# Performance work log

Hardware: AMD Instinct MI355X
Metric: run time of the kernel (lower is better)

Reference implementation:

```python
import jax, jax.numpy as jnp
import numpy as np

N = 100000      # physical-network nodes
E = 3200000     # directed edges (avg degree 32)
DIN = 128       # input_dim
DH = 128        # embedding_dim
DOUT = 128      # output_dim
NUM_GRAPHS = 1


def setup_inputs() -> dict:
    key = jax.random.key(0)
    ks = jax.random.split(key, 8)
    s = 0.05
    x = jax.random.normal(ks[0], (N, DIN), dtype=jnp.float32)
    edge_index = jax.random.randint(ks[1], (2, E), 0, N, dtype=jnp.int64)
    W1 = jax.random.normal(ks[2], (DIN, DH), dtype=jnp.float32) * s
    b1 = jnp.zeros((DH,), dtype=jnp.float32)
    W2 = jax.random.normal(ks[3], (DH, DH), dtype=jnp.float32) * s
    b2 = jnp.zeros((DH,), dtype=jnp.float32)
    W3 = jax.random.normal(ks[4], (DH, DOUT), dtype=jnp.float32) * s
    b3 = jnp.zeros((DOUT,), dtype=jnp.float32)
    return {"x": x, "edge_index": edge_index,
            "W1": W1, "b1": b1, "W2": W2, "b2": b2, "W3": W3, "b3": b3}


def _gcn_norm(edge_index, n_nodes):
    # PyG GCNConv default: add self-loops, symmetric D^{-1/2} (A+I) D^{-1/2} norm.
    loops = jnp.arange(n_nodes, dtype=edge_index.dtype)
    src = jnp.concatenate([edge_index[0], loops])   # [E+N]
    dst = jnp.concatenate([edge_index[1], loops])   # [E+N]
    deg = jax.ops.segment_sum(jnp.ones_like(dst, dtype=jnp.float32), dst,
                              num_segments=n_nodes)
    dinv = jax.lax.rsqrt(deg)  # deg >= 1 because of self-loops
    norm = dinv[src] * dinv[dst]                    # [E+N]
    return src, dst, norm


def _gcn_conv(h, W, b, src, dst, norm, n_nodes):
    h = h @ W                                       # [N, dout] linear first (PyG order)
    msg = h[src] * norm[:, None]                    # gather + edge scaling
    agg = jax.ops.segment_sum(msg, dst, num_segments=n_nodes)  # scatter-add
    return agg + b


def reference(x, edge_index, W1, b1, W2, b2, W3, b3):
    src, dst, norm = _gcn_norm(edge_index, N)
    h = jax.nn.relu(_gcn_conv(x, W1, b1, src, dst, norm, N))
    # dropout is identity in eval mode
    h = jax.nn.relu(_gcn_conv(h, W2, b2, src, dst, norm, N))
    h = _gcn_conv(h, W3, b3, src, dst, norm, N)
    return h.reshape(NUM_GRAPHS, N // NUM_GRAPHS, -1)
```

## Files before the change

kernel.cpp:

```cpp
#include <hip/hip_runtime.h>
#include <cstddef>
#include <cstdint>

#define NN 100000
#define NE 3200000
#define D  128
#define NB 782
#define BSH 7
#define NPB 512
#define CHUNK 6250

typedef short v8s __attribute__((ext_vector_type(8)));
typedef float v4f __attribute__((ext_vector_type(4)));


__device__ __forceinline__ unsigned short f2bf(float f) {
  uint32_t u = __float_as_uint(f);
  uint32_t r = u + 0x7fff + ((u >> 16) & 1);
  return (unsigned short)(r >> 16);
}
__device__ __forceinline__ float bf_lo(uint32_t v) {
  return __uint_as_float(v << 16);
}
__device__ __forceinline__ float bf_hi(uint32_t v) {
  return __uint_as_float(v & 0xffff0000u);
}


__global__ void k_zero(int* __restrict__ p, int n) {
  int i = blockIdx.x * 256 + threadIdx.x;
  if (i < n) p[i] = 0;
}

__global__ __launch_bounds__(256) void kb_count(const int* __restrict__ dst,
                                                int* __restrict__ gb) {
  __shared__ int h[NB];
  for (int i = threadIdx.x; i < NB; i += 256) h[i] = 0;
  __syncthreads();
  int lo = blockIdx.x * CHUNK, hi = lo + CHUNK;
  if (hi > NE) hi = NE;
  for (int e = lo + threadIdx.x; e < hi; e += 256)
    atomicAdd(&h[dst[e] >> BSH], 1);
  __syncthreads();
  for (int i = threadIdx.x; i < NB; i += 256)
    if (h[i]) atomicAdd(&gb[i], h[i]);
}

__global__ __launch_bounds__(1024) void kb_scan(const int* __restrict__ gb,
                                                int* __restrict__ boff,
                                                int* __restrict__ gcur) {
  __shared__ int s[1024];
  int t = threadIdx.x;
  int v = (t < NB) ? gb[t] : 0;
  s[t] = v;
  __syncthreads();
  for (int d = 1; d < 1024; d <<= 1) {
    int u = (t >= d) ? s[t - d] : 0;
    __syncthreads();
    s[t] += u;
    __syncthreads();
  }
  if (t < NB) {
    int x = s[t] - v;
    boff[t] = x;
    gcur[t] = x;
  }
  if (t == 0) boff[NB] = NE;
}

__global__ __launch_bounds__(256) void kb_part(const int* __restrict__ src,
                                               const int* __restrict__ dst,
                                               int* __restrict__ gcur,
                                               uint2* __restrict__ ebuf) {
  __shared__ int h[NB];
  __shared__ int cur[NB];
  for (int i = threadIdx.x; i < NB; i += 256) h[i] = 0;
  __syncthreads();
  int lo = blockIdx.x * CHUNK, hi = lo + CHUNK;
  if (hi > NE) hi = NE;
  for (int e = lo + threadIdx.x; e < hi; e += 256)
    atomicAdd(&h[dst[e] >> BSH], 1);
  __syncthreads();
  for (int i = threadIdx.x; i < NB; i += 256)
    cur[i] = h[i] ? atomicAdd(&gcur[i], h[i]) : 0;
  __syncthreads();
  for (int e = lo + threadIdx.x; e < hi; e += 256) {
    int s = src[e], d = dst[e];
    int p = atomicAdd(&cur[d >> BSH], 1);
    ebuf[p] = make_uint2((unsigned)s, (unsigned)d);
  }
}

__global__ __launch_bounds__(256) void kb_nodecnt(const uint2* __restrict__ ebuf,
                                                  const int* __restrict__ boff,
                                                  int* __restrict__ cnt) {
  int b = blockIdx.x;
  __shared__ int h[128];
  if (threadIdx.x < 128) h[threadIdx.x] = 0;
  __syncthreads();
  int lo = boff[b], hi = boff[b + 1];
  for (int e = lo + threadIdx.x; e < hi; e += 256)
    atomicAdd(&h[ebuf[e].y & 127], 1);
  __syncthreads();
  int node = b * 128 + threadIdx.x;
  if (threadIdx.x < 128 && node < NN) cnt[node] = h[threadIdx.x];
}

__global__ void k_dinv(const int* __restrict__ cnt, float* __restrict__ dinv) {
  int i = blockIdx.x * 256 + threadIdx.x;
  if (i < NN) dinv[i] = rsqrtf((float)(cnt[i] + 1));
}

__global__ void k_scan1(const int* __restrict__ cnt, int* __restrict__ tmp,
                        int* __restrict__ part) {
  __shared__ int s[256];
  int i = blockIdx.x * 256 + threadIdx.x;
  int v = (i < NN) ? cnt[i] : 0;
  s[threadIdx.x] = v;
  __syncthreads();
  for (int d = 1; d < 256; d <<= 1) {
    int t = (threadIdx.x >= d) ? s[threadIdx.x - d] : 0;
    __syncthreads();
    s[threadIdx.x] += t;
    __syncthreads();
  }
  if (i < NN) tmp[i] = s[threadIdx.x] - v;
  if (threadIdx.x == 255) part[blockIdx.x] = s[255];
}

__global__ void k_scan2(int* __restrict__ part, int nb) {
  __shared__ int s[512];
  int v = (threadIdx.x < nb) ? part[threadIdx.x] : 0;
  s[threadIdx.x] = v;
  __syncthreads();
  for (int d = 1; d < 512; d <<= 1) {
    int t = (threadIdx.x >= d) ? s[threadIdx.x - d] : 0;
    __syncthreads();
    s[threadIdx.x] += t;
    __syncthreads();
  }
  if (threadIdx.x < nb) part[threadIdx.x] = s[threadIdx.x] - v;
}

__global__ void k_scan3(const int* __restrict__ tmp, const int* __restrict__ part,
                        int* __restrict__ row_off) {
  int i = blockIdx.x * 256 + threadIdx.x;
  if (i < NN) row_off[i] = tmp[i] + part[blockIdx.x];
  if (blockIdx.x == 0 && threadIdx.x == 0) row_off[NN] = NE;
}

__global__ __launch_bounds__(256) void kb_fill(const uint2* __restrict__ ebuf,
                                               const int* __restrict__ boff,
                                               const int* __restrict__ row_off,
                                               int* __restrict__ col) {
  int b = blockIdx.x;
  __shared__ int cur[128];
  int node = b * 128 + threadIdx.x;
  if (threadIdx.x < 128) cur[threadIdx.x] = (node < NN) ? row_off[node] : 0;
  __syncthreads();
  int lo = boff[b], hi = boff[b + 1];
  for (int e = lo + threadIdx.x; e < hi; e += 256) {
    uint2 p = ebuf[e];
    int pos = atomicAdd(&cur[p.y & 127], 1);
    col[pos] = (int)p.x;
  }
}


__global__ void k_wt(const float* __restrict__ W, unsigned short* __restrict__ wt) {
  int idx = blockIdx.x * 256 + threadIdx.x;
  if (idx >= 16384) return;
  int k = idx >> 7, c = idx & 127;
  float w = W[idx];
  unsigned short hi = f2bf(w);
  float wh = __uint_as_float((uint32_t)hi << 16);
  unsigned short lo = f2bf(w - wh);
  wt[(size_t)c * 128 + k] = hi;
  wt[16384 + (size_t)c * 128 + k] = lo;
}


__global__ void k_cvt(const float* __restrict__ x, unsigned short* __restrict__ xb) {
  const int n4 = NN * D / 4;
  for (int i = blockIdx.x * 256 + threadIdx.x; i < n4; i += gridDim.x * 256) {
    float4 v = ((const float4*)x)[i];
    uint2 o;
    o.x = (uint32_t)f2bf(v.x) | ((uint32_t)f2bf(v.y) << 16);
    o.y = (uint32_t)f2bf(v.z) | ((uint32_t)f2bf(v.w) << 16);
    ((uint2*)xb)[i] = o;
  }
}


__global__ __launch_bounds__(256) void k_gemm_mfma(
    const unsigned short* __restrict__ A, const unsigned short* __restrict__ wt,
    const float* __restrict__ dinv, unsigned short* __restrict__ C) {
  const int wave = threadIdx.x >> 6;
  const int lane = threadIdx.x & 63;
  const int row0 = blockIdx.x * 128 + wave * 32;
  const int rl = lane & 15;
  const int kg = lane >> 4;

  v4f acc[2][8];
#pragma unroll
  for (int t = 0; t < 2; ++t)
#pragma unroll
    for (int ct = 0; ct < 8; ++ct) acc[t][ct] = (v4f){0.f, 0.f, 0.f, 0.f};

  union U { uint4 u; v8s v; };

#pragma unroll
  for (int ks = 0; ks < 4; ++ks) {
    U a[2];
#pragma unroll
    for (int t = 0; t < 2; ++t) {
      int r = row0 + t * 16 + rl;
      if (r >= NN) r = NN - 1;
      a[t].u = *(const uint4*)(A + (size_t)r * D + ks * 32 + kg * 8);
    }
#pragma unroll
    for (int ct = 0; ct < 8; ++ct) {
      U bh, bl;
      size_t wo = (size_t)(ct * 16 + rl) * 128 + ks * 32 + kg * 8;
      bh.u = *(const uint4*)(wt + wo);
      bl.u = *(const uint4*)(wt + 16384 + wo);
      acc[0][ct] = __builtin_amdgcn_mfma_f32_16x16x32_bf16(a[0].v, bh.v, acc[0][ct], 0, 0, 0);
      acc[1][ct] = __builtin_amdgcn_mfma_f32_16x16x32_bf16(a[1].v, bh.v, acc[1][ct], 0, 0, 0);
      acc[0][ct] = __builtin_amdgcn_mfma_f32_16x16x32_bf16(a[0].v, bl.v, acc[0][ct], 0, 0, 0);
      acc[1][ct] = __builtin_amdgcn_mfma_f32_16x16x32_bf16(a[1].v, bl.v, acc[1][ct], 0, 0, 0);
    }
  }

#pragma unroll
  for (int t = 0; t < 2; ++t) {
#pragma unroll
    for (int i = 0; i < 4; ++i) {
      int row = row0 + t * 16 + kg * 4 + i;
      if (row < NN) {
        float dv = dinv[row];
#pragma unroll
        for (int ct = 0; ct < 8; ++ct)
          C[(size_t)row * D + ct * 16 + rl] = f2bf(dv * acc[t][ct][i]);
      }
    }
  }
}


__global__ __launch_bounds__(256) void k_agg(
    const uint32_t* __restrict__ tu, const int* __restrict__ row_off,
    const int* __restrict__ col, const float* __restrict__ dinv,
    const float* __restrict__ bias, uint32_t* __restrict__ outb,
    float* __restrict__ outf, int fin) {
  int g = blockIdx.x * 4 + (threadIdx.x >> 6);
  if (g >= NN) return;
  int lane = threadIdx.x & 63;
  float di = dinv[g];

  uint32_t sv = tu[(size_t)g * 64 + lane];
  float a0 = bf_lo(sv);
  float a1 = bf_hi(sv);

  int e = row_off[g], end = row_off[g + 1];
  for (; e + 8 <= end; e += 8) {
    int s0 = col[e],     s1 = col[e + 1], s2 = col[e + 2], s3 = col[e + 3];
    int s4 = col[e + 4], s5 = col[e + 5], s6 = col[e + 6], s7 = col[e + 7];
    uint32_t v0 = tu[(size_t)s0 * 64 + lane];
    uint32_t v1 = tu[(size_t)s1 * 64 + lane];
    uint32_t v2 = tu[(size_t)s2 * 64 + lane];
    uint32_t v3 = tu[(size_t)s3 * 64 + lane];
    uint32_t v4 = tu[(size_t)s4 * 64 + lane];
    uint32_t v5 = tu[(size_t)s5 * 64 + lane];
    uint32_t v6 = tu[(size_t)s6 * 64 + lane];
    uint32_t v7 = tu[(size_t)s7 * 64 + lane];
    a0 += bf_lo(v0); a1 += bf_hi(v0);
    a0 += bf_lo(v1); a1 += bf_hi(v1);
    a0 += bf_lo(v2); a1 += bf_hi(v2);
    a0 += bf_lo(v3); a1 += bf_hi(v3);
    a0 += bf_lo(v4); a1 += bf_hi(v4);
    a0 += bf_lo(v5); a1 += bf_hi(v5);
    a0 += bf_lo(v6); a1 += bf_hi(v6);
    a0 += bf_lo(v7); a1 += bf_hi(v7);
  }
  for (; e < end; ++e) {
    uint32_t v0 = tu[(size_t)col[e] * 64 + lane];
    a0 += bf_lo(v0); a1 += bf_hi(v0);
  }

  int c = lane * 2;
  float r0 = di * a0 + bias[c];
  float r1 = di * a1 + bias[c + 1];
  if (!fin) {
    r0 = fmaxf(r0, 0.f);
    r1 = fmaxf(r1, 0.f);
    outb[(size_t)g * 64 + lane] = (uint32_t)f2bf(r0) | ((uint32_t)f2bf(r1) << 16);
  } else {
    *(float2*)(outf + (size_t)g * D + c) = make_float2(r0, r1);
  }
}


extern "C" void kernel_launch(void* const* d_in, const int* in_sizes, int n_in,
                              void* d_out, int out_size, void* d_ws, size_t ws_size,
                              hipStream_t stream) {
  const float* x  = (const float*)d_in[0];
  const int*   ei = (const int*)d_in[1];
  const float* W1 = (const float*)d_in[2];
  const float* b1 = (const float*)d_in[3];
  const float* W2 = (const float*)d_in[4];
  const float* b2 = (const float*)d_in[5];
  const float* W3 = (const float*)d_in[6];
  const float* b3 = (const float*)d_in[7];
  float* out = (float*)d_out;

  char* base = (char*)d_ws;
  size_t o = 0;
  auto take = [&](size_t bytes) {
    void* p = base + o;
    o += (bytes + 255) & ~(size_t)255;
    return p;
  };
  int*   cnt     = (int*)take((size_t)NN * 4);
  int*   tmp     = (int*)take((size_t)NN * 4);
  int*   row_off = (int*)take((size_t)(NN + 1) * 4);
  float* dinv    = (float*)take((size_t)NN * 4);
  int*   part    = (int*)take(512 * 4);
  int*   gb      = (int*)take((size_t)NB * 4);
  int*   boff    = (int*)take((size_t)(NB + 1) * 4);
  int*   gcur    = (int*)take((size_t)NB * 4);
  unsigned short* wt1 = (unsigned short*)take(2 * 16384 * 2);
  unsigned short* wt2 = (unsigned short*)take(2 * 16384 * 2);
  unsigned short* wt3 = (unsigned short*)take(2 * 16384 * 2);
  void* region1 = take((size_t)NE * 8);
  int*  col     = (int*)take((size_t)NE * 4);
  unsigned short* t0 = (unsigned short*)take((size_t)NN * D * 2);

  uint2* ebuf = (uint2*)region1;
  unsigned short* xb = (unsigned short*)region1;
  unsigned short* h  = (unsigned short*)region1;

  const int* src = ei;
  const int* dst = ei + NE;

  const int nbN = (NN + 255) / 256;

  k_zero    <<<(NB + 255) / 256, 256, 0, stream>>>(gb, NB);
  kb_count  <<<NPB, 256, 0, stream>>>(dst, gb);
  kb_scan   <<<1, 1024, 0, stream>>>(gb, boff, gcur);
  kb_part   <<<NPB, 256, 0, stream>>>(src, dst, gcur, ebuf);
  kb_nodecnt<<<NB, 256, 0, stream>>>(ebuf, boff, cnt);
  k_dinv    <<<nbN, 256, 0, stream>>>(cnt, dinv);
  k_scan1   <<<nbN, 256, 0, stream>>>(cnt, tmp, part);
  k_scan2   <<<1, 512, 0, stream>>>(part, nbN);
  k_scan3   <<<nbN, 256, 0, stream>>>(tmp, part, row_off);
  kb_fill   <<<NB, 256, 0, stream>>>(ebuf, boff, row_off, col);

  k_wt <<<64, 256, 0, stream>>>(W1, wt1);
  k_wt <<<64, 256, 0, stream>>>(W2, wt2);
  k_wt <<<64, 256, 0, stream>>>(W3, wt3);
  k_cvt<<<2048, 256, 0, stream>>>(x, xb);

  const int gB = (NN + 127) / 128;
  const int aB = (NN + 3) / 4;

  k_gemm_mfma<<<gB, 256, 0, stream>>>(xb, wt1, dinv, t0);
  k_agg<<<aB, 256, 0, stream>>>((const uint32_t*)t0, row_off, col, dinv, b1,
                                (uint32_t*)h, nullptr, 0);
  k_gemm_mfma<<<gB, 256, 0, stream>>>(h, wt2, dinv, t0);
  k_agg<<<aB, 256, 0, stream>>>((const uint32_t*)t0, row_off, col, dinv, b2,
                                (uint32_t*)h, nullptr, 0);
  k_gemm_mfma<<<gB, 256, 0, stream>>>(h, wt3, dinv, t0);
  k_agg<<<aB, 256, 0, stream>>>((const uint32_t*)t0, row_off, col, dinv, b3,
                                nullptr, out, 1);
}
```

Before: 594.7 us.

## Fuse CSR build kernels, drop split-bf16 weights, fold x conversion into GEMM

Merges node counting, degree normalisation, the three-pass scan and the CSR fill into one per-bucket kernel. Each bucket's row offsets come from a local scan plus its bucket base offset. The weight matrices are now stored as a single bf16 copy instead of a hi/lo pair, which halves the MFMA work and weight loads but drops the extra precision term. The separate fp32-to-bf16 conversion pass over x is removed by converting inside a templated GEMM that also doubles the rows per wave. These changes cut launches, removed passes and memory traffic, at the cost of lower weight precision and more registers per wave.

```diff
diff --git a/kernel.cpp b/kernel.cpp
--- a/kernel.cpp
+++ b/kernel.cpp
@@ -91,74 +91,41 @@
   }
 }
 
-__global__ __launch_bounds__(256) void kb_nodecnt(const uint2* __restrict__ ebuf,
-                                                  const int* __restrict__ boff,
-                                                  int* __restrict__ cnt) {
+__global__ __launch_bounds__(256) void kb_build(const uint2* __restrict__ ebuf,
+                                                const int* __restrict__ boff,
+                                                int* __restrict__ row_off,
+                                                float* __restrict__ dinv,
+                                                int* __restrict__ col) {
   int b = blockIdx.x;
   __shared__ int h[128];
+  __shared__ int s[128];
+  __shared__ int cur[128];
   if (threadIdx.x < 128) h[threadIdx.x] = 0;
   __syncthreads();
   int lo = boff[b], hi = boff[b + 1];
   for (int e = lo + threadIdx.x; e < hi; e += 256)
     atomicAdd(&h[ebuf[e].y & 127], 1);
   __syncthreads();
-  int node = b * 128 + threadIdx.x;
-  if (threadIdx.x < 128 && node < NN) cnt[node] = h[threadIdx.x];
-}
-
-__global__ void k_dinv(const int* __restrict__ cnt, float* __restrict__ dinv) {
-  int i = blockIdx.x * 256 + threadIdx.x;
-  if (i < NN) dinv[i] = rsqrtf((float)(cnt[i] + 1));
-}
-
-__global__ void k_scan1(const int* __restrict__ cnt, int* __restrict__ tmp,
-                        int* __restrict__ part) {
-  __shared__ int s[256];
-  int i = blockIdx.x * 256 + threadIdx.x;
-  int v = (i < NN) ? cnt[i] : 0;
-  s[threadIdx.x] = v;
-  __syncthreads();
-  for (int d = 1; d < 256; d <<= 1) {
-    int t = (threadIdx.x >= d) ? s[threadIdx.x - d] : 0;
+  int v = (threadIdx.x < 128) ? h[threadIdx.x] : 0;
+  if (threadIdx.x < 128) s[threadIdx.x] = v;
+  __syncthreads();
+  for (int d = 1; d < 128; d <<= 1) {
+    int t = (threadIdx.x < 128 && threadIdx.x >= d) ? s[threadIdx.x - d] : 0;
     __syncthreads();
-    s[threadIdx.x] += t;
+    if (threadIdx.x < 128) s[threadIdx.x] += t;
     __syncthreads();
   }
-  if (i < NN) tmp[i] = s[threadIdx.x] - v;
-  if (threadIdx.x == 255) part[blockIdx.x] = s[255];
-}
-
-__global__ void k_scan2(int* __restrict__ part, int nb) {
-  __shared__ int s[512];
-  int v = (threadIdx.x < nb) ? part[threadIdx.x] : 0;
-  s[threadIdx.x] = v;
-  __syncthreads();
-  for (int d = 1; d < 512; d <<= 1) {
-    int t = (threadIdx.x >= d) ? s[threadIdx.x - d] : 0;
-    __syncthreads();
-    s[threadIdx.x] += t;
-    __syncthreads();
-  }
-  if (threadIdx.x < nb) part[threadIdx.x] = s[threadIdx.x] - v;
-}
-
-__global__ void k_scan3(const int* __restrict__ tmp, const int* __restrict__ part,
-                        int* __restrict__ row_off) {
-  int i = blockIdx.x * 256 + threadIdx.x;
-  if (i < NN) row_off[i] = tmp[i] + part[blockIdx.x];
-  if (blockIdx.x == 0 && threadIdx.x == 0) row_off[NN] = NE;
-}
-
-__global__ __launch_bounds__(256) void kb_fill(const uint2* __restrict__ ebuf,
-                                               const int* __restrict__ boff,
-                                               const int* __restrict__ row_off,
-                                               int* __restrict__ col) {
-  int b = blockIdx.x;
-  __shared__ int cur[128];
-  int node = b * 128 + threadIdx.x;
-  if (threadIdx.x < 128) cur[threadIdx.x] = (node < NN) ? row_off[node] : 0;
-  __syncthreads();
-  int lo = boff[b], hi = boff[b + 1];
+  if (threadIdx.x < 128) {
+    int ro = lo + s[threadIdx.x] - v;
+    cur[threadIdx.x] = ro;
+    int node = b * 128 + threadIdx.x;
+    if (node < NN) {
+      row_off[node] = ro;
+      dinv[node] = rsqrtf((float)(v + 1));
+    }
+  }
+  if (b == NB - 1 && threadIdx.x == 0) row_off[NN] = NE;
+  __syncthreads();
   for (int e = lo + threadIdx.x; e < hi; e += 256) {
     uint2 p = ebuf[e];
     int pos = atomicAdd(&cur[p.y & 127], 1);
@@ -171,68 +138,62 @@
   int idx = blockIdx.x * 256 + threadIdx.x;
   if (idx >= 16384) return;
   int k = idx >> 7, c = idx & 127;
-  float w = W[idx];
-  unsigned short hi = f2bf(w);
-  float wh = __uint_as_float((uint32_t)hi << 16);
-  unsigned short lo = f2bf(w - wh);
-  wt[(size_t)c * 128 + k] = hi;
-  wt[16384 + (size_t)c * 128 + k] = lo;
-}
-
-
-__global__ void k_cvt(const float* __restrict__ x, unsigned short* __restrict__ xb) {
-  const int n4 = NN * D / 4;
-  for (int i = blockIdx.x * 256 + threadIdx.x; i < n4; i += gridDim.x * 256) {
-    float4 v = ((const float4*)x)[i];
-    uint2 o;
-    o.x = (uint32_t)f2bf(v.x) | ((uint32_t)f2bf(v.y) << 16);
-    o.y = (uint32_t)f2bf(v.z) | ((uint32_t)f2bf(v.w) << 16);
-    ((uint2*)xb)[i] = o;
-  }
-}
-
-
-__global__ __launch_bounds__(256) void k_gemm_mfma(
-    const unsigned short* __restrict__ A, const unsigned short* __restrict__ wt,
-    const float* __restrict__ dinv, unsigned short* __restrict__ C) {
+  wt[(size_t)c * 128 + k] = f2bf(W[idx]);
+}
+
+
+template <int F32IN>
+__global__ __launch_bounds__(256) void k_gemm2(const void* __restrict__ Av,
+                                               const unsigned short* __restrict__ wt,
+                                               const float* __restrict__ dinv,
+                                               unsigned short* __restrict__ C) {
   const int wave = threadIdx.x >> 6;
   const int lane = threadIdx.x & 63;
-  const int row0 = blockIdx.x * 128 + wave * 32;
+  const int row0 = blockIdx.x * 256 + wave * 64;
   const int rl = lane & 15;
   const int kg = lane >> 4;
 
-  v4f acc[2][8];
-#pragma unroll
-  for (int t = 0; t < 2; ++t)
+  v4f acc[4][8];
+#pragma unroll
+  for (int t = 0; t < 4; ++t)
 #pragma unroll
     for (int ct = 0; ct < 8; ++ct) acc[t][ct] = (v4f){0.f, 0.f, 0.f, 0.f};
 
-  union U { uint4 u; v8s v; };
+  union U { uint4 u; v8s v; unsigned short us[8]; };
 
 #pragma unroll
   for (int ks = 0; ks < 4; ++ks) {
-    U a[2];
-#pragma unroll
-    for (int t = 0; t < 2; ++t) {
+    U a[4];
+#pragma unroll
+    for (int t = 0; t < 4; ++t) {
       int r = row0 + t * 16 + rl;
       if (r >= NN) r = NN - 1;
-      a[t].u = *(const uint4*)(A + (size_t)r * D + ks * 32 + kg * 8);
+      if (F32IN) {
+        const float* ap = (const float*)Av + (size_t)r * D + ks * 32 + kg * 8;
+        float4 l4 = *(const float4*)ap;
+        float4 h4 = *(const float4*)(ap + 4);
+        a[t].us[0] = f2bf(l4.x); a[t].us[1] = f2bf(l4.y);
+        a[t].us[2] = f2bf(l4.z); a[t].us[3] = f2bf(l4.w);
+        a[t].us[4] = f2bf(h4.x); a[t].us[5] = f2bf(h4.y);
+        a[t].us[6] = f2bf(h4.z); a[t].us[7] = f2bf(h4.w);
+      } else {
+        a[t].u = *(const uint4*)((const unsigned short*)Av +
+                                 (size_t)r * D + ks * 32 + kg * 8);
+      }
     }
 #pragma unroll
     for (int ct = 0; ct < 8; ++ct) {
-      U bh, bl;
-      size_t wo = (size_t)(ct * 16 + rl) * 128 + ks * 32 + kg * 8;
-      bh.u = *(const uint4*)(wt + wo);
-      bl.u = *(const uint4*)(wt + 16384 + wo);
-      acc[0][ct] = __builtin_amdgcn_mfma_f32_16x16x32_bf16(a[0].v, bh.v, acc[0][ct], 0, 0, 0);
-      acc[1][ct] = __builtin_amdgcn_mfma_f32_16x16x32_bf16(a[1].v, bh.v, acc[1][ct], 0, 0, 0);
-      acc[0][ct] = __builtin_amdgcn_mfma_f32_16x16x32_bf16(a[0].v, bl.v, acc[0][ct], 0, 0, 0);
-      acc[1][ct] = __builtin_amdgcn_mfma_f32_16x16x32_bf16(a[1].v, bl.v, acc[1][ct], 0, 0, 0);
+      U b;
+      b.u = *(const uint4*)(wt + (size_t)(ct * 16 + rl) * 128 + ks * 32 + kg * 8);
+#pragma unroll
+      for (int t = 0; t < 4; ++t)
+        acc[t][ct] =
+            __builtin_amdgcn_mfma_f32_16x16x32_bf16(a[t].v, b.v, acc[t][ct], 0, 0, 0);
     }
   }
 
 #pragma unroll
-  for (int t = 0; t < 2; ++t) {
+  for (int t = 0; t < 4; ++t) {
 #pragma unroll
     for (int i = 0; i < 4; ++i) {
       int row = row0 + t * 16 + kg * 4 + i;
@@ -320,56 +281,44 @@
     o += (bytes + 255) & ~(size_t)255;
     return p;
   };
-  int*   cnt     = (int*)take((size_t)NN * 4);
-  int*   tmp     = (int*)take((size_t)NN * 4);
   int*   row_off = (int*)take((size_t)(NN + 1) * 4);
   float* dinv    = (float*)take((size_t)NN * 4);
-  int*   part    = (int*)take(512 * 4);
   int*   gb      = (int*)take((size_t)NB * 4);
   int*   boff    = (int*)take((size_t)(NB + 1) * 4);
   int*   gcur    = (int*)take((size_t)NB * 4);
-  unsigned short* wt1 = (unsigned short*)take(2 * 16384 * 2);
-  unsigned short* wt2 = (unsigned short*)take(2 * 16384 * 2);
-  unsigned short* wt3 = (unsigned short*)take(2 * 16384 * 2);
+  unsigned short* wt1 = (unsigned short*)take(16384 * 2);
+  unsigned short* wt2 = (unsigned short*)take(16384 * 2);
+  unsigned short* wt3 = (unsigned short*)take(16384 * 2);
   void* region1 = take((size_t)NE * 8);
   int*  col     = (int*)take((size_t)NE * 4);
   unsigned short* t0 = (unsigned short*)take((size_t)NN * D * 2);
 
   uint2* ebuf = (uint2*)region1;
-  unsigned short* xb = (unsigned short*)region1;
-  unsigned short* h  = (unsigned short*)region1;
+  unsigned short* h = (unsigned short*)region1;
 
   const int* src = ei;
   const int* dst = ei + NE;
 
-  const int nbN = (NN + 255) / 256;
-
-  k_zero    <<<(NB + 255) / 256, 256, 0, stream>>>(gb, NB);
-  kb_count  <<<NPB, 256, 0, stream>>>(dst, gb);
-  kb_scan   <<<1, 1024, 0, stream>>>(gb, boff, gcur);
-  kb_part   <<<NPB, 256, 0, stream>>>(src, dst, gcur, ebuf);
-  kb_nodecnt<<<NB, 256, 0, stream>>>(ebuf, boff, cnt);
-  k_dinv    <<<nbN, 256, 0, stream>>>(cnt, dinv);
-  k_scan1   <<<nbN, 256, 0, stream>>>(cnt, tmp, part);
-  k_scan2   <<<1, 512, 0, stream>>>(part, nbN);
-  k_scan3   <<<nbN, 256, 0, stream>>>(tmp, part, row_off);
-  kb_fill   <<<NB, 256, 0, stream>>>(ebuf, boff, row_off, col);
-
-  k_wt <<<64, 256, 0, stream>>>(W1, wt1);
-  k_wt <<<64, 256, 0, stream>>>(W2, wt2);
-  k_wt <<<64, 256, 0, stream>>>(W3, wt3);
-  k_cvt<<<2048, 256, 0, stream>>>(x, xb);
-
-  const int gB = (NN + 127) / 128;
+  k_zero  <<<(NB + 255) / 256, 256, 0, stream>>>(gb, NB);
+  kb_count<<<NPB, 256, 0, stream>>>(dst, gb);
+  kb_scan <<<1, 1024, 0, stream>>>(gb, boff, gcur);
+  kb_part <<<NPB, 256, 0, stream>>>(src, dst, gcur, ebuf);
+  kb_build<<<NB, 256, 0, stream>>>(ebuf, boff, row_off, dinv, col);
+
+  k_wt<<<64, 256, 0, stream>>>(W1, wt1);
+  k_wt<<<64, 256, 0, stream>>>(W2, wt2);
+  k_wt<<<64, 256, 0, stream>>>(W3, wt3);
+
+  const int gB = (NN + 255) / 256;
   const int aB = (NN + 3) / 4;
 
-  k_gemm_mfma<<<gB, 256, 0, stream>>>(xb, wt1, dinv, t0);
+  k_gemm2<1><<<gB, 256, 0, stream>>>(x, wt1, dinv, t0);
   k_agg<<<aB, 256, 0, stream>>>((const uint32_t*)t0, row_off, col, dinv, b1,
                                 (uint32_t*)h, nullptr, 0);
-  k_gemm_mfma<<<gB, 256, 0, stream>>>(h, wt2, dinv, t0);
+  k_gemm2<0><<<gB, 256, 0, stream>>>(h, wt2, dinv, t0);
   k_agg<<<aB, 256, 0, stream>>>((const uint32_t*)t0, row_off, col, dinv, b2,
                                 (uint32_t*)h, nullptr, 0);
-  k_gemm_mfma<<<gB, 256, 0, stream>>>(h, wt3, dinv, t0);
+  k_gemm2<0><<<gB, 256, 0, stream>>>(h, wt3, dinv, t0);
   k_agg<<<aB, 256, 0, stream>>>((const uint32_t*)t0, row_off, col, dinv, b3,
                                 nullptr, out, 1);
 }
```

New measurement: 512.6 us. 1.16x faster.
